# Performance work log

Hardware: AMD Instinct MI355X
Metric: run time of the kernel (lower is better)

Reference implementation:

```python
import jax, jax.numpy as jnp
import numpy as np

B, S, HID, NH = 8, 1024, 1024, 16
DH = HID // NH
ZERO = 1e-8  # undefined repo constant, assumed small epsilon


def setup_inputs() -> dict:
    key = jax.random.key(0)
    ks = jax.random.split(key, 14)
    sc = 1.0 / np.sqrt(HID)
    inp = {
        "Q": jax.random.normal(ks[0], (B, S, HID), jnp.float32),
        "K": jax.random.normal(ks[1], (B, S, HID), jnp.float32),
        "V": jax.random.normal(ks[2], (B, S, HID), jnp.float32),
        "Q_mask": jax.random.randint(ks[3], (B, S), 0, 2).astype(jnp.float32),
        "K_mask": jax.random.randint(ks[4], (B, S), 0, 2).astype(jnp.float32),
        "Wq": jax.random.normal(ks[5], (HID, HID), jnp.float32) * sc,
        "bq": jnp.zeros((HID,), jnp.float32),
        "Wk": jax.random.normal(ks[6], (HID, HID), jnp.float32) * sc,
        "bk": jnp.zeros((HID,), jnp.float32),
        "Wv": jax.random.normal(ks[7], (HID, HID), jnp.float32) * sc,
        "bv": jnp.zeros((HID,), jnp.float32),
        "Wo": jax.random.normal(ks[8], (HID, HID), jnp.float32) * sc,
        "bo": jnp.zeros((HID,), jnp.float32),
    }
    return inp


def _heads(x):  # [B,S,HID] -> [B,NH,S,DH]
    b, s, _ = x.shape
    return x.reshape(b, s, NH, DH).transpose(0, 2, 1, 3)


def reference(Q, K, V, Q_mask, K_mask, Wq, bq, Wk, bk, Wv, bv, Wo, bo):
    q = _heads(Q @ Wq.T + bq)
    k = _heads(K @ Wk.T + bk)
    v = _heads(V @ Wv.T + bv)
    # NOTE: original divides by head_size**(-0.5) == multiply by sqrt(DH)
    scores = jnp.einsum("bhqd,bhkd->bhqk", q, k) / (DH ** (-0.5))
    mask = Q_mask[:, :, None] * K_mask[:, None, :]  # [B,Sq,Sk]
    probs = jax.nn.softmax(scores, axis=-1)
    probs = jnp.where(mask[:, None, :, :] == 0, 0.0, probs)
    probs = probs / jnp.sum(probs + ZERO, axis=-1, keepdims=True)
    ctx = jnp.einsum("bhqk,bhkd->bqhd", probs, v).reshape(Q.shape[0], Q.shape[1], HID)
    return ctx @ Wo.T + bo
```

## Files before the change

### kernel.cpp

```cpp
#include <hip/hip_runtime.h>
#include <math.h>

constexpr int Bc   = 8;
constexpr int Sc   = 1024;
constexpr int HIDc = 1024;
constexpr int NHc  = 16;
constexpr int DHc  = 64;
constexpr int Mc   = Bc * Sc;
constexpr int Kc2  = 1024;
constexpr float SCALE    = 8.0f;
constexpr float EPS_TERM = 1024.0f * 1e-8f;

typedef short s16x8 __attribute__((ext_vector_type(8)));
typedef float f32x4 __attribute__((ext_vector_type(4)));

__device__ __forceinline__ ushort f2bf(float f) {
  unsigned u = __float_as_uint(f);
  u += 0x7FFFu + ((u >> 16) & 1u);
  return (ushort)(u >> 16);
}
__device__ __forceinline__ float bf2f(ushort h) {
  return __uint_as_float(((unsigned)h) << 16);
}
__device__ __forceinline__ unsigned pk2bf(float a, float b) {
  return (unsigned)f2bf(a) | ((unsigned)f2bf(b) << 16);
}

__device__ __forceinline__ void gl_lds16(const ushort* g, ushort* l) {
  __builtin_amdgcn_global_load_lds(
      (const __attribute__((address_space(1))) void*)g,
      (__attribute__((address_space(3))) void*)l, 16, 0, 0);
}

__device__ __forceinline__ void split8(const float4 v0, const float4 v1,
                                       s16x8& hi, s16x8& lo) {
  const float f[8] = {v0.x, v0.y, v0.z, v0.w, v1.x, v1.y, v1.z, v1.w};
  ushort h[8], l[8];
#pragma unroll
  for (int i = 0; i < 8; i++) {
    h[i] = f2bf(f[i]);
    l[i] = f2bf(f[i] - bf2f(h[i]));
  }
#pragma unroll
  for (int i = 0; i < 8; i++) { hi[i] = (short)h[i]; lo[i] = (short)l[i]; }
}

__global__ __launch_bounds__(256) void cvt_all(
    const float4* __restrict__ Wq, const float4* __restrict__ Wk,
    const float4* __restrict__ Wv, const float4* __restrict__ Wo,
    ushort4* __restrict__ Wqh, ushort4* __restrict__ Wql,
    ushort4* __restrict__ Wkh, ushort4* __restrict__ Wkl,
    ushort4* __restrict__ Wvh, ushort4* __restrict__ Woh,
    const float4* __restrict__ Qf, const float4* __restrict__ Kf,
    const float4* __restrict__ Vf,
    s16x8* __restrict__ Qsh, s16x8* __restrict__ Qsl,
    s16x8* __restrict__ Ksh, s16x8* __restrict__ Ksl,
    s16x8* __restrict__ Vsh)
{
  const int bid = blockIdx.x;
  if (bid < 4096) {
    const int seg = bid >> 10;
    const int li  = (bid & 1023) * 256 + threadIdx.x;
    if (seg == 0) {
      const float4 v = Wq[li];
      ushort4 h, l;
      h.x = f2bf(v.x); l.x = f2bf(v.x - bf2f(h.x));
      h.y = f2bf(v.y); l.y = f2bf(v.y - bf2f(h.y));
      h.z = f2bf(v.z); l.z = f2bf(v.z - bf2f(h.z));
      h.w = f2bf(v.w); l.w = f2bf(v.w - bf2f(h.w));
      Wqh[li] = h; Wql[li] = l;
    } else if (seg == 1) {
      const float4 v = Wk[li];
      ushort4 h, l;
      h.x = f2bf(v.x); l.x = f2bf(v.x - bf2f(h.x));
      h.y = f2bf(v.y); l.y = f2bf(v.y - bf2f(h.y));
      h.z = f2bf(v.z); l.z = f2bf(v.z - bf2f(h.z));
      h.w = f2bf(v.w); l.w = f2bf(v.w - bf2f(h.w));
      Wkh[li] = h; Wkl[li] = l;
    } else {
      const float4 v = (seg == 2) ? Wv[li] : Wo[li];
      ushort4 h;
      h.x = f2bf(v.x); h.y = f2bf(v.y); h.z = f2bf(v.z); h.w = f2bf(v.w);
      if (seg == 2) Wvh[li] = h; else Woh[li] = h;
    }
  } else {
    const int r   = bid - 4096;
    const int seg = r >> 12;
    const int li  = (r & 4095) * 256 + threadIdx.x;
    const float4* src = (seg == 0) ? Qf : (seg == 1) ? Kf : Vf;
    const float4 v0 = src[2 * li];
    const float4 v1 = src[2 * li + 1];
    if (seg < 2) {
      s16x8 hi, lo;
      split8(v0, v1, hi, lo);
      if (seg == 0) { Qsh[li] = hi; Qsl[li] = lo; }
      else          { Ksh[li] = hi; Ksl[li] = lo; }
    } else {
      const float f[8] = {v0.x, v0.y, v0.z, v0.w, v1.x, v1.y, v1.z, v1.w};
      s16x8 hi;
#pragma unroll
      for (int i = 0; i < 8; i++) hi[i] = (short)f2bf(f[i]);
      Vsh[li] = hi;
    }
  }
}

__global__ __launch_bounds__(256, 2) void qkv_gemm(
    const ushort* __restrict__ Qsh, const ushort* __restrict__ Qsl,
    const ushort* __restrict__ Ksh, const ushort* __restrict__ Ksl,
    const ushort* __restrict__ Vsh,
    const ushort* __restrict__ Wqh, const ushort* __restrict__ Wql,
    const ushort* __restrict__ Wkh, const ushort* __restrict__ Wkl,
    const ushort* __restrict__ Wvh,
    const float* __restrict__ bq, const float* __restrict__ bk,
    const float* __restrict__ bv,
    ushort* __restrict__ qhi, ushort* __restrict__ qlo,
    ushort* __restrict__ khi, ushort* __restrict__ klo,
    ushort* __restrict__ vt)
{
  __shared__ ushort AhL[2][4096];
  __shared__ ushort BhL[2][4096];
  __shared__ ushort AlL[2][4096];
  __shared__ ushort BlL[2][4096];

  const int bid = blockIdx.x;
  const int wid = (bid & 7) * 192 + (bid >> 3);
  const int z   = wid >> 9;
  const int rem = wid & 511;
  const int m0  = (rem >> 3) * 128;
  const int n0  = (rem & 7) * 128;

  const bool split = (z < 2);
  const ushort* Ah = (z == 0) ? Qsh : (z == 1) ? Ksh : Vsh;
  const ushort* Al = (z == 0) ? Qsl : Ksl;
  const ushort* Bh = (z == 0) ? Wqh : (z == 1) ? Wkh : Wvh;
  const ushort* Bl = (z == 0) ? Wql : Wkl;
  const float* bias = (z == 0) ? bq : (z == 1) ? bk : bv;

  const int t    = threadIdx.x;
  const int w    = t >> 6;
  const int ln   = t & 63;
  const int col  = ln & 15;
  const int quad = ln >> 4;
  const int wm   = w >> 1, wn = w & 1;

  f32x4 acc[4][4] = {};

  const int sA = w * 128;

  auto STAGE = [&](int buf, int k0) {
#pragma unroll
    for (int j = 0; j < 2; j++) {
      const int s = sA + j * 64 + ln;
      const int r = s & 127, c = s >> 7;
      const int ldst = (sA + j * 64) * 8;
      const size_t goA = (size_t)(m0 + r) * Kc2 + k0 + c * 8;
      const size_t goB = (size_t)(n0 + r) * Kc2 + k0 + c * 8;
      gl_lds16(Ah + goA, &AhL[buf][ldst]);
      gl_lds16(Bh + goB, &BhL[buf][ldst]);
      if (split) {
        gl_lds16(Al + goA, &AlL[buf][ldst]);
        gl_lds16(Bl + goB, &BlL[buf][ldst]);
      }
    }
  };

  auto COMPUTE = [&](int buf) {
    s16x8 a_h[4], b_h[4], a_l[4], b_l[4];
#pragma unroll
    for (int i = 0; i < 4; i++) {
      const int ai = (quad * 128 + wm * 64 + i * 16 + col) * 8;
      const int bi = (quad * 128 + wn * 64 + i * 16 + col) * 8;
      a_h[i] = *(const s16x8*)&AhL[buf][ai];
      b_h[i] = *(const s16x8*)&BhL[buf][bi];
      if (split) {
        a_l[i] = *(const s16x8*)&AlL[buf][ai];
        b_l[i] = *(const s16x8*)&BlL[buf][bi];
      }
    }
#pragma unroll
    for (int i = 0; i < 4; i++)
#pragma unroll
      for (int jj = 0; jj < 4; jj++) {
        acc[i][jj] = __builtin_amdgcn_mfma_f32_16x16x32_bf16(a_h[i], b_h[jj], acc[i][jj], 0, 0, 0);
        if (split) {
          acc[i][jj] = __builtin_amdgcn_mfma_f32_16x16x32_bf16(a_h[i], b_l[jj], acc[i][jj], 0, 0, 0);
          acc[i][jj] = __builtin_amdgcn_mfma_f32_16x16x32_bf16(a_l[i], b_h[jj], acc[i][jj], 0, 0, 0);
        }
      }
  };

  STAGE(0, 0);
  __syncthreads();
  int cur = 0;
  for (int kt = 0; kt < 31; ++kt) {
    STAGE(cur ^ 1, (kt + 1) * 32);
    COMPUTE(cur);
    __syncthreads();
    cur ^= 1;
  }
  COMPUTE(cur);

  const int mb = m0 + wm * 64;
  const int nb = n0 + wn * 64;
  ushort* Ch = (z == 0) ? qhi : khi;
  ushort* Cl = (z == 0) ? qlo : klo;
#pragma unroll
  for (int i = 0; i < 4; i++)
#pragma unroll
    for (int jj = 0; jj < 4; jj++) {
      const int n  = nb + jj * 16 + col;
      const float bvv = bias[n];
#pragma unroll
      for (int r = 0; r < 4; r++) {
        const int m   = mb + i * 16 + quad * 4 + r;
        const float v = acc[i][jj][r] + bvv;
        const int b_ = m >> 10, s = m & (Sc - 1);
        const int h_ = n >> 6,  d = n & (DHc - 1);
        if (split) {
          const size_t off = (((size_t)b_ * NHc + h_) * Sc + s) * DHc + d;
          const ushort hb = f2bf(v);
          Ch[off] = hb;
          Cl[off] = f2bf(v - bf2f(hb));
        } else {
          const size_t off = (((size_t)b_ * NHc + h_) * DHc + d) * Sc + s;
          vt[off] = f2bf(v);
        }
      }
    }
}

__global__ __launch_bounds__(256, 3) void o_gemm(
    const ushort* __restrict__ Ag, const ushort* __restrict__ Bg,
    const float* __restrict__ bias, float* __restrict__ C)
{
  __shared__ ushort AhL[2][4096];
  __shared__ ushort BhL[2][4096];

  const int bid = blockIdx.x;
  const int wid = (bid & 7) * 64 + (bid >> 3);
  const int m0  = (wid >> 3) * 128;
  const int n0  = (wid & 7) * 128;

  const int t    = threadIdx.x;
  const int w    = t >> 6;
  const int ln   = t & 63;
  const int col  = ln & 15;
  const int quad = ln >> 4;
  const int wm   = w >> 1, wn = w & 1;

  f32x4 acc[4][4] = {};
  const int sA = w * 128;

  auto STAGE = [&](int buf, int k0) {
#pragma unroll
    for (int j = 0; j < 2; j++) {
      const int s = sA + j * 64 + ln;
      const int r = s & 127, c = s >> 7;
      const int ldst = (sA + j * 64) * 8;
      gl_lds16(Ag + (size_t)(m0 + r) * Kc2 + k0 + c * 8, &AhL[buf][ldst]);
      gl_lds16(Bg + (size_t)(n0 + r) * Kc2 + k0 + c * 8, &BhL[buf][ldst]);
    }
  };

  auto COMPUTE = [&](int buf) {
    s16x8 a_h[4], b_h[4];
#pragma unroll
    for (int i = 0; i < 4; i++) {
      a_h[i] = *(const s16x8*)&AhL[buf][(quad * 128 + wm * 64 + i * 16 + col) * 8];
      b_h[i] = *(const s16x8*)&BhL[buf][(quad * 128 + wn * 64 + i * 16 + col) * 8];
    }
#pragma unroll
    for (int i = 0; i < 4; i++)
#pragma unroll
      for (int jj = 0; jj < 4; jj++)
        acc[i][jj] = __builtin_amdgcn_mfma_f32_16x16x32_bf16(a_h[i], b_h[jj], acc[i][jj], 0, 0, 0);
  };

  STAGE(0, 0);
  __syncthreads();
  int cur = 0;
  for (int kt = 0; kt < 31; ++kt) {
    STAGE(cur ^ 1, (kt + 1) * 32);
    COMPUTE(cur);
    __syncthreads();
    cur ^= 1;
  }
  COMPUTE(cur);

  const int mb = m0 + wm * 64;
  const int nb = n0 + wn * 64;
#pragma unroll
  for (int i = 0; i < 4; i++)
#pragma unroll
    for (int jj = 0; jj < 4; jj++) {
      const int n  = nb + jj * 16 + col;
      const float bvv = bias[n];
#pragma unroll
      for (int r = 0; r < 4; r++) {
        const int m = mb + i * 16 + quad * 4 + r;
        C[(size_t)m * HIDc + n] = acc[i][jj][r] + bvv;
      }
    }
}

constexpr int LDP = 72;

__global__ __launch_bounds__(256, 4) void attn_mfma(
    const ushort* __restrict__ qhi, const ushort* __restrict__ qlo,
    const ushort* __restrict__ khi, const ushort* __restrict__ klo,
    const ushort* __restrict__ vt,  const float* __restrict__ Qm,
    const float* __restrict__ Km,   ushort* __restrict__ ctx)
{
  __shared__ ushort KhiL[4096];
  __shared__ ushort KloL[4096];
  __shared__ ushort VtL [4096];
  __shared__ ushort PmL [64 * LDP];
  __shared__ float  kmL[64];

  const int t    = threadIdx.x;
  const int w    = t >> 6;
  const int ln   = t & 63;
  const int col  = ln & 15;
  const int quad = ln >> 4;

  const int id  = blockIdx.x;
  const int xcd = id & 7;
  const int j   = id >> 3;
  const int bh  = xcd * 16 + (j >> 4);
  const int qt  = j & 15;
  const int b   = bh >> 4;
  const int h   = bh & 15;

  const int qbase = qt * 64 + w * 16;
  const size_t headoff = (size_t)bh * Sc * DHc;

  s16x8 qh0, qh1, ql0, ql1;
  {
    const size_t ro = headoff + (size_t)(qbase + col) * DHc + quad * 8;
    qh0 = *(const s16x8*)(qhi + ro);
    qh1 = *(const s16x8*)(qhi + ro + 32);
    ql0 = *(const s16x8*)(qlo + ro);
    ql1 = *(const s16x8*)(qlo + ro + 32);
  }

  f32x4 OT[4] = {{0,0,0,0},{0,0,0,0},{0,0,0,0},{0,0,0,0}};
  float mrow = -INFINITY;
  float Zp = 0.0f, Zmp = 0.0f;

  for (int k0 = 0; k0 < Sc; k0 += 64) {
    __syncthreads();
#pragma unroll
    for (int jj = 0; jj < 2; jj++) {
      const int c = jj * 4 + w;
      const size_t gk = headoff + (size_t)(k0 + ln) * DHc + c * 8;
      const size_t gv = headoff + (size_t)ln * Sc + k0 + c * 8;
      gl_lds16(khi + gk, &KhiL[c * 512]);
      gl_lds16(klo + gk, &KloL[c * 512]);
      gl_lds16(vt  + gv, &VtL [c * 512]);
    }
    if (t < 64) kmL[t] = Km[b * Sc + k0 + t];
    __syncthreads();

    float s[4][4];
    __builtin_amdgcn_s_setprio(1);
#pragma unroll
    for (int ks = 0; ks < 4; ks++) {
      const int base0 = (quad * 64 + ks * 16 + col) * 8;
      const int base1 = ((quad + 4) * 64 + ks * 16 + col) * 8;
      const s16x8 kh0 = *(const s16x8*)&KhiL[base0];
      const s16x8 kh1 = *(const s16x8*)&KhiL[base1];
      const s16x8 kl0 = *(const s16x8*)&KloL[base0];
      const s16x8 kl1 = *(const s16x8*)&KloL[base1];
      f32x4 a = {0,0,0,0};
      a = __builtin_amdgcn_mfma_f32_16x16x32_bf16(kh0, qh0, a, 0, 0, 0);
      a = __builtin_amdgcn_mfma_f32_16x16x32_bf16(kh1, qh1, a, 0, 0, 0);
      a = __builtin_amdgcn_mfma_f32_16x16x32_bf16(kh0, ql0, a, 0, 0, 0);
      a = __builtin_amdgcn_mfma_f32_16x16x32_bf16(kh1, ql1, a, 0, 0, 0);
      a = __builtin_amdgcn_mfma_f32_16x16x32_bf16(kl0, qh0, a, 0, 0, 0);
      a = __builtin_amdgcn_mfma_f32_16x16x32_bf16(kl1, qh1, a, 0, 0, 0);
#pragma unroll
      for (int r = 0; r < 4; r++) s[ks][r] = a[r] * SCALE;
    }
    __builtin_amdgcn_s_setprio(0);

    float tmax = s[0][0];
#pragma unroll
    for (int ks = 0; ks < 4; ks++)
#pragma unroll
      for (int r = 0; r < 4; r++) tmax = fmaxf(tmax, s[ks][r]);
    tmax = fmaxf(tmax, __shfl_xor(tmax, 16, 64));
    tmax = fmaxf(tmax, __shfl_xor(tmax, 32, 64));

    float mn;
    const bool defer = __all(tmax - mrow <= 8.0f);
    if (defer) {
      mn = mrow;
    } else {
      mn = fmaxf(mrow, tmax);
      const float alpha = __expf(mrow - mn);
      mrow = mn;
      Zp  *= alpha;
      Zmp *= alpha;
#pragma unroll
      for (int dt = 0; dt < 4; dt++) OT[dt] *= alpha;
    }

    float ps = 0.0f, pms = 0.0f;
    const int prow = (w * 16 + col) * LDP;
#pragma unroll
    for (int ks = 0; ks < 4; ks++) {
      const float4 km4 = *(const float4*)&kmL[ks * 16 + quad * 4];
      const float p0 = __expf(s[ks][0] - mn), p1 = __expf(s[ks][1] - mn);
      const float p2 = __expf(s[ks][2] - mn), p3 = __expf(s[ks][3] - mn);
      const float q0 = p0 * km4.x, q1 = p1 * km4.y, q2 = p2 * km4.z, q3 = p3 * km4.w;
      ps  += (p0 + p1) + (p2 + p3);
      pms += (q0 + q1) + (q2 + q3);
      uint2 pv;
      pv.x = pk2bf(q0, q1);
      pv.y = pk2bf(q2, q3);
      *(uint2*)&PmL[prow + ks * 16 + quad * 4] = pv;
    }
    Zp  += ps;
    Zmp += pms;

    const s16x8 p0 = *(const s16x8*)&PmL[prow + quad * 8];
    const s16x8 p1 = *(const s16x8*)&PmL[prow + 32 + quad * 8];
    __builtin_amdgcn_s_setprio(1);
#pragma unroll
    for (int dt = 0; dt < 4; dt++) {
      const s16x8 a0 = *(const s16x8*)&VtL[(quad * 64 + dt * 16 + col) * 8];
      const s16x8 a1 = *(const s16x8*)&VtL[((quad + 4) * 64 + dt * 16 + col) * 8];
      OT[dt] = __builtin_amdgcn_mfma_f32_16x16x32_bf16(a0, p0, OT[dt], 0, 0, 0);
      OT[dt] = __builtin_amdgcn_mfma_f32_16x16x32_bf16(a1, p1, OT[dt], 0, 0, 0);
    }
    __builtin_amdgcn_s_setprio(0);
  }

  Zp  += __shfl_xor(Zp,  16, 64);  Zp  += __shfl_xor(Zp,  32, 64);
  Zmp += __shfl_xor(Zmp, 16, 64);  Zmp += __shfl_xor(Zmp, 32, 64);

  const int q     = qbase + col;
  const float qmv = Qm[b * Sc + q];
  const float rden = (qmv != 0.0f) ? 1.0f / (Zmp + EPS_TERM * Zp) : 0.0f;

  ushort* crow = ctx + (size_t)(b * Sc + q) * HIDc + h * DHc + quad * 4;
#pragma unroll
  for (int dt = 0; dt < 4; dt++) {
    uint2 ov;
    ov.x = pk2bf(OT[dt][0] * rden, OT[dt][1] * rden);
    ov.y = pk2bf(OT[dt][2] * rden, OT[dt][3] * rden);
    *(uint2*)(crow + dt * 16) = ov;
  }
}

extern "C" void kernel_launch(void* const* d_in, const int* in_sizes, int n_in,
                              void* d_out, int out_size, void* d_ws, size_t ws_size,
                              hipStream_t stream)
{
  const float* Q  = (const float*)d_in[0];
  const float* K  = (const float*)d_in[1];
  const float* V  = (const float*)d_in[2];
  const float* Qm = (const float*)d_in[3];
  const float* Km = (const float*)d_in[4];
  const float* Wq = (const float*)d_in[5];
  const float* bq = (const float*)d_in[6];
  const float* Wk = (const float*)d_in[7];
  const float* bk = (const float*)d_in[8];
  const float* Wv = (const float*)d_in[9];
  const float* bv = (const float*)d_in[10];
  const float* Wo = (const float*)d_in[11];
  const float* bo = (const float*)d_in[12];
  float* out = (float*)d_out;

  const size_t NEL = (size_t)Mc * HIDc;
  const size_t WEL = (size_t)HIDc * HIDc;

  ushort* Wqh = (ushort*)d_ws;
  ushort* Wql = Wqh + WEL;
  ushort* Wkh = Wql + WEL;
  ushort* Wkl = Wkh + WEL;
  ushort* Wvh = Wkl + WEL;
  ushort* Woh = Wvh + WEL;
  ushort* Qsh = Woh + WEL;
  ushort* Qsl = Qsh + NEL;
  ushort* Ksh = Qsl + NEL;
  ushort* Ksl = Ksh + NEL;
  ushort* Vsh = Ksl + NEL;
  ushort* qhi = Vsh + NEL;
  ushort* qlo = qhi + NEL;
  ushort* khi = qlo + NEL;
  ushort* klo = khi + NEL;
  ushort* vt  = klo + NEL;
  ushort* ctx = Qsh;

  cvt_all<<<16384, 256, 0, stream>>>(
      (const float4*)Wq, (const float4*)Wk, (const float4*)Wv, (const float4*)Wo,
      (ushort4*)Wqh, (ushort4*)Wql, (ushort4*)Wkh, (ushort4*)Wkl,
      (ushort4*)Wvh, (ushort4*)Woh,
      (const float4*)Q, (const float4*)K, (const float4*)V,
      (s16x8*)Qsh, (s16x8*)Qsl, (s16x8*)Ksh, (s16x8*)Ksl, (s16x8*)Vsh);

  qkv_gemm<<<dim3(3 * (Mc / 128) * (HIDc / 128)), 256, 0, stream>>>(
      Qsh, Qsl, Ksh, Ksl, Vsh,
      Wqh, Wql, Wkh, Wkl, Wvh, bq, bk, bv, qhi, qlo, khi, klo, vt);

  attn_mfma<<<Bc * NHc * (Sc / 64), 256, 0, stream>>>(qhi, qlo, khi, klo, vt, Qm, Km, ctx);

  o_gemm<<<dim3((Mc / 128) * (HIDc / 128)), 256, 0, stream>>>(ctx, Woh, bo, out);
}
```

Before: 526.2 us.

## Enlarge QKV GEMM tile to 256x128 with 512 threads, single-buffered LDS

The QKV projection GEMM now uses 512-thread blocks computing 256x128 output tiles, so each staged weight tile is shared by twice as many rows and the grid is halved. To fit shared memory, the double-buffered LDS staging is replaced by a single buffer with a sync before and after each load. This aims to cut global traffic for the weight operand and raise per-block reuse, but it gives up the overlap of loads with MFMA compute. Each K-step now waits on its own load, so latency is exposed.

```diff
diff --git a/kernel.cpp b/kernel.cpp
--- a/kernel.cpp
+++ b/kernel.cpp
@@ -105,7 +105,7 @@
   }
 }
 
-__global__ __launch_bounds__(256, 2) void qkv_gemm(
+__global__ __launch_bounds__(512, 2) void qkv_gemm(
     const ushort* __restrict__ Qsh, const ushort* __restrict__ Qsl,
     const ushort* __restrict__ Ksh, const ushort* __restrict__ Ksl,
     const ushort* __restrict__ Vsh,
@@ -118,16 +118,16 @@
     ushort* __restrict__ khi, ushort* __restrict__ klo,
     ushort* __restrict__ vt)
 {
-  __shared__ ushort AhL[2][4096];
-  __shared__ ushort BhL[2][4096];
-  __shared__ ushort AlL[2][4096];
-  __shared__ ushort BlL[2][4096];
+  __shared__ ushort AhL[8192];
+  __shared__ ushort AlL[8192];
+  __shared__ ushort BhL[4096];
+  __shared__ ushort BlL[4096];
 
   const int bid = blockIdx.x;
-  const int wid = (bid & 7) * 192 + (bid >> 3);
-  const int z   = wid >> 9;
-  const int rem = wid & 511;
-  const int m0  = (rem >> 3) * 128;
+  const int wid = (bid & 7) * 96 + (bid >> 3);
+  const int z   = wid >> 8;
+  const int rem = wid & 255;
+  const int m0  = (rem >> 3) * 256;
   const int n0  = (rem & 7) * 128;
 
   const bool split = (z < 2);
@@ -142,40 +142,41 @@
   const int ln   = t & 63;
   const int col  = ln & 15;
   const int quad = ln >> 4;
-  const int wm   = w >> 1, wn = w & 1;
+  const int wm   = w >> 1;
+  const int wn   = w & 1;
 
   f32x4 acc[4][4] = {};
 
-  const int sA = w * 128;
-
-  auto STAGE = [&](int buf, int k0) {
+  auto STAGE = [&](int k0) {
 #pragma unroll
     for (int j = 0; j < 2; j++) {
-      const int s = sA + j * 64 + ln;
-      const int r = s & 127, c = s >> 7;
-      const int ldst = (sA + j * 64) * 8;
+      const int g = j * 512 + w * 64 + ln;
+      const int r = g & 255, c = g >> 8;
       const size_t goA = (size_t)(m0 + r) * Kc2 + k0 + c * 8;
+      ushort* dA = &AhL[(size_t)(j * 512 + w * 64) * 8];
+      gl_lds16(Ah + goA, dA);
+      if (split) gl_lds16(Al + goA, &AlL[(size_t)(j * 512 + w * 64) * 8]);
+    }
+    {
+      const int g = w * 64 + ln;
+      const int r = g & 127, c = g >> 7;
       const size_t goB = (size_t)(n0 + r) * Kc2 + k0 + c * 8;
-      gl_lds16(Ah + goA, &AhL[buf][ldst]);
-      gl_lds16(Bh + goB, &BhL[buf][ldst]);
+      gl_lds16(Bh + goB, &BhL[(size_t)(w * 64) * 8]);
+      if (split) gl_lds16(Bl + goB, &BlL[(size_t)(w * 64) * 8]);
+    }
+  };
+
+  auto COMPUTE = [&]() {
+    s16x8 a_h[4], b_h[4], a_l[4], b_l[4];
+#pragma unroll
+    for (int i = 0; i < 4; i++) {
+      const int ai = (quad * 256 + wm * 64 + i * 16 + col) * 8;
+      const int bi = (quad * 128 + wn * 64 + i * 16 + col) * 8;
+      a_h[i] = *(const s16x8*)&AhL[ai];
+      b_h[i] = *(const s16x8*)&BhL[bi];
       if (split) {
-        gl_lds16(Al + goA, &AlL[buf][ldst]);
-        gl_lds16(Bl + goB, &BlL[buf][ldst]);
-      }
-    }
-  };
-
-  auto COMPUTE = [&](int buf) {
-    s16x8 a_h[4], b_h[4], a_l[4], b_l[4];
-#pragma unroll
-    for (int i = 0; i < 4; i++) {
-      const int ai = (quad * 128 + wm * 64 + i * 16 + col) * 8;
-      const int bi = (quad * 128 + wn * 64 + i * 16 + col) * 8;
-      a_h[i] = *(const s16x8*)&AhL[buf][ai];
-      b_h[i] = *(const s16x8*)&BhL[buf][bi];
-      if (split) {
-        a_l[i] = *(const s16x8*)&AlL[buf][ai];
-        b_l[i] = *(const s16x8*)&BlL[buf][bi];
+        a_l[i] = *(const s16x8*)&AlL[ai];
+        b_l[i] = *(const s16x8*)&BlL[bi];
       }
     }
 #pragma unroll
@@ -190,16 +191,12 @@
       }
   };
 
-  STAGE(0, 0);
-  __syncthreads();
-  int cur = 0;
-  for (int kt = 0; kt < 31; ++kt) {
-    STAGE(cur ^ 1, (kt + 1) * 32);
-    COMPUTE(cur);
+  for (int k0 = 0; k0 < Kc2; k0 += 32) {
     __syncthreads();
-    cur ^= 1;
-  }
-  COMPUTE(cur);
+    STAGE(k0);
+    __syncthreads();
+    COMPUTE();
+  }
 
   const int mb = m0 + wm * 64;
   const int nb = n0 + wn * 64;
@@ -501,7 +498,7 @@
       (const float4*)Q, (const float4*)K, (const float4*)V,
       (s16x8*)Qsh, (s16x8*)Qsl, (s16x8*)Ksh, (s16x8*)Ksl, (s16x8*)Vsh);
 
-  qkv_gemm<<<dim3(3 * (Mc / 128) * (HIDc / 128)), 256, 0, stream>>>(
+  qkv_gemm<<<dim3(3 * (Mc / 256) * (HIDc / 128)), 512, 0, stream>>>(
       Qsh, Qsl, Ksh, Ksl, Vsh,
       Wqh, Wql, Wkh, Wkl, Wvh, bq, bk, bv, qhi, qlo, khi, klo, vt);
 
```

After: 626.5 us. 19.1% more time.
